# Optimization experiments

Measured on AMD Instinct MI355X. Metric: run time of the kernel, lower is better.

## Reference

```python
import jax, jax.numpy as jnp
import numpy as np

E = 8          # num_experts
K = 2          # top_k
CAPF = 1.25    # capacity_factor


def setup_inputs() -> dict:
    key = jax.random.key(0)
    ks = jax.random.split(key, 6)
    B, T, C = 4, 2048, 1024
    x = jax.random.normal(ks[0], (B, T, C), jnp.float32)
    noise = jax.random.normal(ks[1], (B, T, E), jnp.float32)  # stands in for torch.randn_like
    Wr = jax.random.normal(ks[2], (C, E), jnp.float32) * 0.02   # topkroute_linear
    Wn = jax.random.normal(ks[3], (C, E), jnp.float32) * 0.02   # noise_linear
    W1 = jax.random.normal(ks[4], (E, C, 4 * C), jnp.float32) * 0.02  # expert up-proj
    W2 = jax.random.normal(ks[5], (E, 4 * C, C), jnp.float32) * 0.02  # expert down-proj
    return {"x": x, "noise": noise, "Wr": Wr, "Wn": Wn, "W1": W1, "W2": W2}


def reference(x, noise, Wr, Wn, W1, W2):
    B, T, C = x.shape
    N = B * T
    cap = int(N * K / E * CAPF)  # expert_capacity (static)

    # --- NoisyTopkRouter ---
    logits = x @ Wr                                  # [B,T,E]
    noise_logits = x @ Wn                            # [B,T,E]
    noisy = logits + noise * jax.nn.softplus(noise_logits)
    _, idx = jax.lax.top_k(noisy, K)                 # [B,T,K]
    mask_bte = (idx[..., None] == jnp.arange(E)).any(axis=-2)       # [B,T,E]
    gating = jax.nn.softmax(jnp.where(mask_bte, noisy, -jnp.inf), axis=-1)

    flat_x = x.reshape(N, C)
    flat_g = gating.reshape(N, E)

    # --- capacity-limited dispatch (token order, first `cap` per expert) ---
    mask = mask_bte.reshape(N, E).T                  # [E,N]
    rank = jnp.cumsum(mask, axis=1) - 1              # position within expert
    keep = mask & (rank < cap)
    slot = jnp.where(keep, rank, cap)                # overflow -> dump slot `cap`
    tok = jnp.where(keep, jnp.arange(N)[None, :], N) # dropped -> pad token `N`
    s2t = jnp.full((E, cap + 1), N, dtype=jnp.int32)
    s2t = s2t.at[jnp.arange(E)[:, None], slot].set(tok.astype(jnp.int32))[:, :cap]  # [E,cap]

    # --- gather, grouped GEMM (Linear-SiLU-Linear), weight, scatter-add ---
    x_pad = jnp.concatenate([flat_x, jnp.zeros((1, C), flat_x.dtype)], axis=0)
    xin = x_pad[s2t]                                 # [E,cap,C]
    h = jax.nn.silu(jnp.einsum('enc,ech->enh', xin, W1))
    out = jnp.einsum('enh,ehc->enc', h, W2)          # [E,cap,C]
    g_pad = jnp.concatenate([flat_g, jnp.zeros((1, E), flat_g.dtype)], axis=0)
    gate = g_pad[s2t, jnp.arange(E)[:, None]]        # [E,cap]
    weighted = out * gate[..., None]
    upd = jnp.zeros((N + 1, C), x.dtype).at[s2t.reshape(-1)].add(weighted.reshape(-1, C))
    return upd[:N].reshape(B, T, C)
```

## Files before the change

kernel.cpp:

```cpp
#include <hip/hip_runtime.h>
#include <hip/hip_bf16.h>
#include <math.h>

#define C_DIM 1024
#define H_DIM 4096
#define E_NUM 8

typedef __bf16 bf16x8 __attribute__((ext_vector_type(8)));
typedef float f32x4 __attribute__((ext_vector_type(4)));

__device__ __forceinline__ unsigned short f2bf(float f) {
  union { float f; unsigned u; } v; v.f = f;
  unsigned r = v.u + 0x7FFFu + ((v.u >> 16) & 1u);
  return (unsigned short)(r >> 16);
}

__device__ __forceinline__ void gload16(const short* g, short* l) {
  __builtin_amdgcn_global_load_lds(
      (const __attribute__((address_space(1))) unsigned int*)g,
      (__attribute__((address_space(3))) unsigned int*)l, 16, 0, 0);
}

__global__ __launch_bounds__(256) void router_kernel(
    const float* __restrict__ x, const float* __restrict__ noise,
    const float* __restrict__ Wr, const float* __restrict__ Wn,
    int2* __restrict__ idx_out, float2* __restrict__ gate_out, int N)
{
  int t = blockIdx.x;
  int tid = threadIdx.x;
  const float* xrow = x + (size_t)t * C_DIM;
  float accR[E_NUM], accN[E_NUM];
#pragma unroll
  for (int e = 0; e < E_NUM; e++) { accR[e] = 0.f; accN[e] = 0.f; }
  for (int c = tid; c < C_DIM; c += 256) {
    float xv = xrow[c];
    const float* wr = Wr + (size_t)c * E_NUM;
    const float* wn = Wn + (size_t)c * E_NUM;
#pragma unroll
    for (int e = 0; e < E_NUM; e++) {
      accR[e] = fmaf(xv, wr[e], accR[e]);
      accN[e] = fmaf(xv, wn[e], accN[e]);
    }
  }
#pragma unroll
  for (int e = 0; e < E_NUM; e++) {
    for (int off = 32; off > 0; off >>= 1) {
      accR[e] += __shfl_down(accR[e], off, 64);
      accN[e] += __shfl_down(accN[e], off, 64);
    }
  }
  __shared__ float red[4][2 * E_NUM];
  int lane = tid & 63, wave = tid >> 6;
  if (lane == 0) {
#pragma unroll
    for (int e = 0; e < E_NUM; e++) { red[wave][e] = accR[e]; red[wave][E_NUM + e] = accN[e]; }
  }
  __syncthreads();
  if (tid == 0) {
    float ns[E_NUM];
#pragma unroll
    for (int e = 0; e < E_NUM; e++) {
      float lg = red[0][e] + red[1][e] + red[2][e] + red[3][e];
      float nl = red[0][E_NUM + e] + red[1][E_NUM + e] + red[2][E_NUM + e] + red[3][E_NUM + e];
      float sp = fmaxf(nl, 0.f) + log1pf(expf(-fabsf(nl)));
      ns[e] = lg + noise[(size_t)t * E_NUM + e] * sp;
    }
    int i1 = 0; float m1 = ns[0];
    int i2 = -1; float m2 = -INFINITY;
#pragma unroll
    for (int e = 1; e < E_NUM; e++) {
      float v = ns[e];
      if (v > m1) { m2 = m1; i2 = i1; m1 = v; i1 = e; }
      else if (v > m2) { m2 = v; i2 = e; }
    }
    float e2 = expf(m2 - m1);
    float s = 1.f + e2;
    gate_out[t] = make_float2(1.f / s, e2 / s);
    idx_out[t] = make_int2(i1, i2);
  }
}

__global__ __launch_bounds__(256) void scan_kernel(
    const int2* __restrict__ idx, const float2* __restrict__ gates,
    int* __restrict__ s2t, float* __restrict__ gslot, int N, int cap)
{
  int e = blockIdx.x;
  int tid = threadIdx.x;
  for (int s = tid; s < cap; s += 256) { s2t[(size_t)e * cap + s] = N; gslot[(size_t)e * cap + s] = 0.f; }
  __syncthreads();
  __shared__ int wtot[4];
  int lane = tid & 63, wave = tid >> 6;
  int running = 0;
  for (int base = 0; base < N; base += 256) {
    int t = base + tid;
    int2 ix = idx[t];
    bool flag = (ix.x == e) || (ix.y == e);
    unsigned long long m = __ballot(flag);
    int rank = __popcll(m & ((1ull << lane) - 1ull));
    if (lane == 0) wtot[wave] = __popcll(m);
    __syncthreads();
    int woff = 0;
    for (int w = 0; w < wave; w++) woff += wtot[w];
    int slot = running + woff + rank;
    if (flag && slot < cap) {
      s2t[(size_t)e * cap + slot] = t;
      gslot[(size_t)e * cap + slot] = (ix.x == e) ? gates[t].x : gates[t].y;
    }
    running += wtot[0] + wtot[1] + wtot[2] + wtot[3];
    __syncthreads();
  }
}

__global__ __launch_bounds__(256) void convert_x_kernel(
    const float* __restrict__ src, short* __restrict__ dst, int n8)
{
  int i = blockIdx.x * 256 + threadIdx.x;
  if (i >= n8) return;
  const float4* s = (const float4*)src + (size_t)i * 2;
  float4 a = s[0], b = s[1];
  union { unsigned short us[8]; uint4 v; } o;
  o.us[0] = f2bf(a.x); o.us[1] = f2bf(a.y); o.us[2] = f2bf(a.z); o.us[3] = f2bf(a.w);
  o.us[4] = f2bf(b.x); o.us[5] = f2bf(b.y); o.us[6] = f2bf(b.z); o.us[7] = f2bf(b.w);
  ((uint4*)dst)[i] = o.v;
}

__global__ __launch_bounds__(256) void transpose_convert_kernel(
    const float* __restrict__ src, short* __restrict__ dst,
    int R, int Cc, int eBase)
{
  src += (size_t)(eBase + blockIdx.z) * R * Cc;
  dst += (size_t)blockIdx.z * (size_t)R * Cc;
  __shared__ float tile[64][65];
  int c0 = blockIdx.x * 64, r0 = blockIdx.y * 64;
  int tid = threadIdx.x;
  int tr = tid >> 4, tc = (tid & 15) * 4;
#pragma unroll
  for (int p = 0; p < 4; p++) {
    int r = p * 16 + tr;
    float4 v = *(const float4*)(src + (size_t)(r0 + r) * Cc + c0 + tc);
    tile[r][tc] = v.x; tile[r][tc + 1] = v.y; tile[r][tc + 2] = v.z; tile[r][tc + 3] = v.w;
  }
  __syncthreads();
#pragma unroll
  for (int p = 0; p < 4; p++) {
    int c = p * 16 + tr;
    union { unsigned short us[4]; ushort4 v; } o;
#pragma unroll
    for (int j = 0; j < 4; j++) o.us[j] = f2bf(tile[tc + j][c]);
    *(ushort4*)(dst + (size_t)(c0 + c) * R + r0 + tc) = o.v;
  }
}

__global__ __launch_bounds__(256) void mlp1_kernel(
    const short* __restrict__ xbf, const short* __restrict__ W1t,
    const int* __restrict__ s2t, short* __restrict__ h,
    int eBase, int cap, int N)
{
  int ez = blockIdx.z;
  int e = eBase + ez;
  const short* Wt = W1t + (size_t)ez * C_DIM * H_DIM;
  short* hE = h + (size_t)ez * (size_t)cap * H_DIM;
  int row0 = blockIdx.y * 128;
  int col0 = blockIdx.x * 128;
  int tid = threadIdx.x;
  int w = tid >> 6, lane = tid & 63;

  __shared__ short As[4096];
  __shared__ short Bs[4096];

  int tokA = min(s2t[(size_t)e * cap + row0 + lane], N - 1);
  int tokB = min(s2t[(size_t)e * cap + row0 + 64 + lane], N - 1);
  const short* pA0 = xbf + (size_t)tokA * C_DIM + w * 8;
  const short* pA1 = xbf + (size_t)tokB * C_DIM + w * 8;
  const short* pB0 = Wt + (size_t)(col0 + lane) * C_DIM + w * 8;
  const short* pB1 = Wt + (size_t)(col0 + 64 + lane) * C_DIM + w * 8;
  short* lA0 = &As[w * 1024];
  short* lA1 = &As[w * 1024 + 512];
  short* lB0 = &Bs[w * 1024];
  short* lB1 = &Bs[w * 1024 + 512];

  int wr = w >> 1, wc = w & 1;
  int fr = lane & 15, fb = lane >> 4;
  int aoff = (fb * 128 + wr * 64 + fr) * 8;
  int boff = (fb * 128 + wc * 64 + fr) * 8;

  f32x4 acc[4][4];
#pragma unroll
  for (int m = 0; m < 4; m++)
#pragma unroll
    for (int n = 0; n < 4; n++) acc[m][n] = 0.f;

  for (int k0 = 0; k0 < C_DIM; k0 += 32) {
    gload16(pA0 + k0, lA0);
    gload16(pA1 + k0, lA1);
    gload16(pB0 + k0, lB0);
    gload16(pB1 + k0, lB1);
    __syncthreads();
    bf16x8 af[4], bg[4];
#pragma unroll
    for (int m = 0; m < 4; m++) af[m] = *(const bf16x8*)&As[aoff + m * 128];
#pragma unroll
    for (int n = 0; n < 4; n++) bg[n] = *(const bf16x8*)&Bs[boff + n * 128];
#pragma unroll
    for (int m = 0; m < 4; m++)
#pragma unroll
      for (int n = 0; n < 4; n++)
        acc[m][n] = __builtin_amdgcn_mfma_f32_16x16x32_bf16(af[m], bg[n], acc[m][n], 0, 0, 0);
    __syncthreads();
  }
  int orow = row0 + wr * 64 + fb * 4;
  int ocol = col0 + wc * 64 + fr;
#pragma unroll
  for (int m = 0; m < 4; m++)
#pragma unroll
    for (int r = 0; r < 4; r++) {
      size_t rbase = (size_t)(orow + m * 16 + r) * H_DIM + ocol;
#pragma unroll
      for (int n = 0; n < 4; n++) {
        float v = acc[m][n][r];
        hE[rbase + n * 16] = (short)f2bf(v / (1.f + expf(-v)));
      }
    }
}

__global__ __launch_bounds__(256) void mlp2_kernel(
    const short* __restrict__ h, const short* __restrict__ W2t,
    const int* __restrict__ s2t, const float* __restrict__ gslot,
    float* __restrict__ out, int eBase, int cap, int N)
{
  int ez = blockIdx.z;
  int e = eBase + ez;
  const short* A = h + (size_t)ez * (size_t)cap * H_DIM;
  const short* Wt = W2t + (size_t)ez * C_DIM * H_DIM;
  int row0 = blockIdx.y * 128;
  int col0 = blockIdx.x * 128;
  int tid = threadIdx.x;
  int w = tid >> 6, lane = tid & 63;

  __shared__ short As[4096];
  __shared__ short Bs[4096];

  const short* pA0 = A + (size_t)(row0 + lane) * H_DIM + w * 8;
  const short* pA1 = A + (size_t)(row0 + 64 + lane) * H_DIM + w * 8;
  const short* pB0 = Wt + (size_t)(col0 + lane) * H_DIM + w * 8;
  const short* pB1 = Wt + (size_t)(col0 + 64 + lane) * H_DIM + w * 8;
  short* lA0 = &As[w * 1024];
  short* lA1 = &As[w * 1024 + 512];
  short* lB0 = &Bs[w * 1024];
  short* lB1 = &Bs[w * 1024 + 512];

  int wr = w >> 1, wc = w & 1;
  int fr = lane & 15, fb = lane >> 4;
  int aoff = (fb * 128 + wr * 64 + fr) * 8;
  int boff = (fb * 128 + wc * 64 + fr) * 8;

  f32x4 acc[4][4];
#pragma unroll
  for (int m = 0; m < 4; m++)
#pragma unroll
    for (int n = 0; n < 4; n++) acc[m][n] = 0.f;

  for (int k0 = 0; k0 < H_DIM; k0 += 32) {
    gload16(pA0 + k0, lA0);
    gload16(pA1 + k0, lA1);
    gload16(pB0 + k0, lB0);
    gload16(pB1 + k0, lB1);
    __syncthreads();
    bf16x8 af[4], bg[4];
#pragma unroll
    for (int m = 0; m < 4; m++) af[m] = *(const bf16x8*)&As[aoff + m * 128];
#pragma unroll
    for (int n = 0; n < 4; n++) bg[n] = *(const bf16x8*)&Bs[boff + n * 128];
#pragma unroll
    for (int m = 0; m < 4; m++)
#pragma unroll
      for (int n = 0; n < 4; n++)
        acc[m][n] = __builtin_amdgcn_mfma_f32_16x16x32_bf16(af[m], bg[n], acc[m][n], 0, 0, 0);
    __syncthreads();
  }
  int ocol = col0 + wc * 64 + fr;
#pragma unroll
  for (int m = 0; m < 4; m++)
#pragma unroll
    for (int r = 0; r < 4; r++) {
      int slot = row0 + wr * 64 + m * 16 + fb * 4 + r;
      int tok = s2t[(size_t)e * cap + slot];
      if (tok < N) {
        float g = gslot[(size_t)e * cap + slot];
        float* op = out + (size_t)tok * C_DIM + ocol;
#pragma unroll
        for (int n = 0; n < 4; n++)
          atomicAdd(op + n * 16, g * acc[m][n][r]);
      }
    }
}

extern "C" void kernel_launch(void* const* d_in, const int* in_sizes, int n_in,
                              void* d_out, int out_size, void* d_ws, size_t ws_size,
                              hipStream_t stream)
{
  const float* x     = (const float*)d_in[0];
  const float* noise = (const float*)d_in[1];
  const float* Wr    = (const float*)d_in[2];
  const float* Wn    = (const float*)d_in[3];
  const float* W1    = (const float*)d_in[4];
  const float* W2    = (const float*)d_in[5];
  float* out = (float*)d_out;

  int N = in_sizes[0] / C_DIM;
  int cap = (int)((double)N * 2.0 / E_NUM * 1.25);

  size_t off = 0;
  auto alloc = [&](size_t bytes) -> char* {
    char* r = (char*)d_ws + off;
    off += (bytes + 255) & ~(size_t)255;
    return r;
  };
  int2*   idx   = (int2*)alloc((size_t)N * sizeof(int2));
  float2* gates = (float2*)alloc((size_t)N * sizeof(float2));
  int*    s2t   = (int*)alloc((size_t)E_NUM * cap * sizeof(int));
  float*  gslot = (float*)alloc((size_t)E_NUM * cap * sizeof(float));
  short*  xbf   = (short*)alloc((size_t)N * C_DIM * sizeof(short));
  size_t fixed = off;

  size_t wBytes = (size_t)C_DIM * H_DIM * sizeof(short);
  size_t hBytes = (size_t)cap * H_DIM * sizeof(short);
  size_t perE = 2 * ((wBytes + 255) & ~(size_t)255) + ((hBytes + 255) & ~(size_t)255);
  int g = (ws_size > fixed) ? (int)((ws_size - fixed) / perE) : 1;
  if (g < 1) g = 1;
  if (g > E_NUM) g = E_NUM;
  short* W1t = (short*)alloc((size_t)g * wBytes);
  short* W2t = (short*)alloc((size_t)g * wBytes);
  short* h   = (short*)alloc((size_t)g * hBytes);

  hipMemsetAsync(d_out, 0, (size_t)out_size * sizeof(float), stream);
  router_kernel<<<N, 256, 0, stream>>>(x, noise, Wr, Wn, idx, gates, N);
  scan_kernel<<<E_NUM, 256, 0, stream>>>(idx, gates, s2t, gslot, N, cap);
  convert_x_kernel<<<(N * C_DIM / 8 + 255) / 256, 256, 0, stream>>>(x, xbf, N * C_DIM / 8);

  for (int eb = 0; eb < E_NUM; eb += g) {
    int ge = min(g, E_NUM - eb);
    transpose_convert_kernel<<<dim3(H_DIM / 64, C_DIM / 64, ge), 256, 0, stream>>>(
        W1, W1t, C_DIM, H_DIM, eb);
    transpose_convert_kernel<<<dim3(C_DIM / 64, H_DIM / 64, ge), 256, 0, stream>>>(
        W2, W2t, H_DIM, C_DIM, eb);
    mlp1_kernel<<<dim3(H_DIM / 128, cap / 128, ge), 256, 0, stream>>>(
        xbf, W1t, s2t, h, eb, cap, N);
    mlp2_kernel<<<dim3(C_DIM / 128, cap / 128, ge), 256, 0, stream>>>(
        h, W2t, s2t, gslot, out, eb, cap, N);
  }
}
```

Baseline: 903.5 us.

## Replace MoE GEMMs with pipelined 256x256 tiled kernel, split-K, and count-based skipping

Merges the two expert GEMM kernels into one templated kernel. It uses 256x256 tiles with 512 threads, a four-buffer LDS pipeline with explicit vmcnt waits and setprio, and XCD-aware block swizzling. Workgroups whose row range lies past an expert's actual token count exit early. The second GEMM is split four ways along K, relying on the existing atomic scatter-add. Weight transposes now run for all experts at once instead of in workspace-limited groups, which needs more workspace and assumes cap is divisible by 256.

```diff
diff --git a/kernel.cpp b/kernel.cpp
--- a/kernel.cpp
+++ b/kernel.cpp
@@ -82,7 +82,8 @@
 
 __global__ __launch_bounds__(256) void scan_kernel(
     const int2* __restrict__ idx, const float2* __restrict__ gates,
-    int* __restrict__ s2t, float* __restrict__ gslot, int N, int cap)
+    int* __restrict__ s2t, float* __restrict__ gslot, int* __restrict__ counts,
+    int N, int cap)
 {
   int e = blockIdx.x;
   int tid = threadIdx.x;
@@ -109,6 +110,7 @@
     running += wtot[0] + wtot[1] + wtot[2] + wtot[3];
     __syncthreads();
   }
+  if (tid == 0) counts[e] = min(running, cap);
 }
 
 __global__ __launch_bounds__(256) void convert_x_kernel(
@@ -126,9 +128,9 @@
 
 __global__ __launch_bounds__(256) void transpose_convert_kernel(
     const float* __restrict__ src, short* __restrict__ dst,
-    int R, int Cc, int eBase)
-{
-  src += (size_t)(eBase + blockIdx.z) * R * Cc;
+    int R, int Cc)
+{
+  src += (size_t)blockIdx.z * R * Cc;
   dst += (size_t)blockIdx.z * (size_t)R * Cc;
   __shared__ float tile[64][65];
   int c0 = blockIdx.x * 64, r0 = blockIdx.y * 64;
@@ -151,148 +153,154 @@
   }
 }
 
-__global__ __launch_bounds__(256) void mlp1_kernel(
-    const short* __restrict__ xbf, const short* __restrict__ W1t,
-    const int* __restrict__ s2t, short* __restrict__ h,
-    int eBase, int cap, int N)
-{
-  int ez = blockIdx.z;
-  int e = eBase + ez;
-  const short* Wt = W1t + (size_t)ez * C_DIM * H_DIM;
-  short* hE = h + (size_t)ez * (size_t)cap * H_DIM;
-  int row0 = blockIdx.y * 128;
-  int col0 = blockIdx.x * 128;
+#define TILE_SH 8192
+
+template<int MODE>
+__global__ __launch_bounds__(512, 2) void gemm_moe(
+    const short* __restrict__ Abase, const short* __restrict__ Wt,
+    const int* __restrict__ s2t, const float* __restrict__ gslot,
+    const int* __restrict__ counts, void* __restrict__ outp,
+    int cap, int N, int rows)
+{
+  __shared__ short As[4 * TILE_SH];
+  __shared__ short Bs[4 * TILE_SH];
+
+  int nwg = gridDim.x;
+  int cpx = nwg >> 3;
+  int flat = blockIdx.x;
+  int swz = (flat & 7) * cpx + (flat >> 3);
+
+  int row, col, e, kc;
+  if (MODE == 0) {
+    row = swz % rows; int tmp = swz / rows;
+    col = tmp & 15; e = tmp >> 4; kc = 0;
+  } else {
+    row = swz % rows; int tmp = swz / rows;
+    col = tmp & 3; tmp >>= 2;
+    kc = tmp & 3; e = tmp >> 2;
+  }
+  int cnt = counts[e];
+  int row0 = row * 256;
+  if (row0 >= cnt) return;
+  int col0 = col * 256;
+
   int tid = threadIdx.x;
-  int w = tid >> 6, lane = tid & 63;
-
-  __shared__ short As[4096];
-  __shared__ short Bs[4096];
-
-  int tokA = min(s2t[(size_t)e * cap + row0 + lane], N - 1);
-  int tokB = min(s2t[(size_t)e * cap + row0 + 64 + lane], N - 1);
-  const short* pA0 = xbf + (size_t)tokA * C_DIM + w * 8;
-  const short* pA1 = xbf + (size_t)tokB * C_DIM + w * 8;
-  const short* pB0 = Wt + (size_t)(col0 + lane) * C_DIM + w * 8;
-  const short* pB1 = Wt + (size_t)(col0 + 64 + lane) * C_DIM + w * 8;
-  short* lA0 = &As[w * 1024];
-  short* lA1 = &As[w * 1024 + 512];
-  short* lB0 = &Bs[w * 1024];
-  short* lB1 = &Bs[w * 1024 + 512];
-
-  int wr = w >> 1, wc = w & 1;
-  int fr = lane & 15, fb = lane >> 4;
-  int aoff = (fb * 128 + wr * 64 + fr) * 8;
-  int boff = (fb * 128 + wc * 64 + fr) * 8;
-
-  f32x4 acc[4][4];
-#pragma unroll
-  for (int m = 0; m < 4; m++)
+  int w = tid >> 6, l = tid & 63;
+  int wr = w >> 2, wc = w & 3;
+  int srow = (w & 3) * 64 + l;
+  int ko0 = (w >> 2) * 8;
+  int ko1 = (2 + (w >> 2)) * 8;
+  int ld0 = (w * 64 + l) * 8;
+  int ld1 = (512 + w * 64 + l) * 8;
+
+  const short* gA;
+  const short* gB;
+  if (MODE == 0) {
+    int tok = s2t[(size_t)e * cap + row0 + srow];
+    if (tok >= N) tok = N - 1;
+    gA = Abase + (size_t)tok * C_DIM;
+    gB = Wt + (size_t)e * (C_DIM * H_DIM) + (size_t)(col0 + srow) * C_DIM;
+  } else {
+    gA = Abase + ((size_t)e * cap + row0 + srow) * H_DIM + kc * 1024;
+    gB = Wt + (size_t)e * (C_DIM * H_DIM) + (size_t)(col0 + srow) * H_DIM + kc * 1024;
+  }
+  const int KT = 32;
+
+  int aBase = ((l >> 4) * 256 + wr * 128 + (l & 15)) * 8;
+  int bBase = ((l >> 4) * 256 + wc * 64 + (l & 15)) * 8;
+
+  f32x4 acc[8][4];
+#pragma unroll
+  for (int m = 0; m < 8; m++)
 #pragma unroll
     for (int n = 0; n < 4; n++) acc[m][n] = 0.f;
 
-  for (int k0 = 0; k0 < C_DIM; k0 += 32) {
-    gload16(pA0 + k0, lA0);
-    gload16(pA1 + k0, lA1);
-    gload16(pB0 + k0, lB0);
-    gload16(pB1 + k0, lB1);
-    __syncthreads();
-    bf16x8 af[4], bg[4];
-#pragma unroll
-    for (int m = 0; m < 4; m++) af[m] = *(const bf16x8*)&As[aoff + m * 128];
-#pragma unroll
-    for (int n = 0; n < 4; n++) bg[n] = *(const bf16x8*)&Bs[boff + n * 128];
+#pragma unroll
+  for (int t = 0; t < 3; ++t) {
+    int boff = t * TILE_SH;
+    gload16(gA + t * 32 + ko0, &As[boff + ld0]);
+    gload16(gA + t * 32 + ko1, &As[boff + ld1]);
+    gload16(gB + t * 32 + ko0, &Bs[boff + ld0]);
+    gload16(gB + t * 32 + ko1, &Bs[boff + ld1]);
+  }
+
+#pragma unroll 1
+  for (int t = 0; t < KT; ++t) {
+    if (t < KT - 2)       asm volatile("s_waitcnt vmcnt(8)" ::: "memory");
+    else if (t == KT - 2) asm volatile("s_waitcnt vmcnt(4)" ::: "memory");
+    else                  asm volatile("s_waitcnt vmcnt(0)" ::: "memory");
+    __builtin_amdgcn_s_barrier();
+    __builtin_amdgcn_sched_barrier(0);
+
+    int bufc = (t & 3) * TILE_SH;
+    int tp = t + 3;
+    int bufp = (tp & 3) * TILE_SH;
+    bool st = tp < KT;
+
+    if (st) {
+      gload16(gA + tp * 32 + ko0, &As[bufp + ld0]);
+      gload16(gA + tp * 32 + ko1, &As[bufp + ld1]);
+    }
+    bf16x8 bfr[4], afr[4];
+#pragma unroll
+    for (int n = 0; n < 4; n++) bfr[n] = *(const bf16x8*)&Bs[bufc + bBase + n * 128];
+#pragma unroll
+    for (int m = 0; m < 4; m++) afr[m] = *(const bf16x8*)&As[bufc + aBase + m * 128];
+    __builtin_amdgcn_s_setprio(1);
 #pragma unroll
     for (int m = 0; m < 4; m++)
 #pragma unroll
       for (int n = 0; n < 4; n++)
-        acc[m][n] = __builtin_amdgcn_mfma_f32_16x16x32_bf16(af[m], bg[n], acc[m][n], 0, 0, 0);
-    __syncthreads();
-  }
-  int orow = row0 + wr * 64 + fb * 4;
-  int ocol = col0 + wc * 64 + fr;
-#pragma unroll
-  for (int m = 0; m < 4; m++)
-#pragma unroll
-    for (int r = 0; r < 4; r++) {
-      size_t rbase = (size_t)(orow + m * 16 + r) * H_DIM + ocol;
-#pragma unroll
-      for (int n = 0; n < 4; n++) {
-        float v = acc[m][n][r];
-        hE[rbase + n * 16] = (short)f2bf(v / (1.f + expf(-v)));
+        acc[m][n] = __builtin_amdgcn_mfma_f32_16x16x32_bf16(afr[m], bfr[n], acc[m][n], 0, 0, 0);
+    __builtin_amdgcn_s_setprio(0);
+
+    if (st) {
+      gload16(gB + tp * 32 + ko0, &Bs[bufp + ld0]);
+      gload16(gB + tp * 32 + ko1, &Bs[bufp + ld1]);
+    }
+#pragma unroll
+    for (int m = 0; m < 4; m++) afr[m] = *(const bf16x8*)&As[bufc + aBase + (m + 4) * 128];
+    __builtin_amdgcn_s_setprio(1);
+#pragma unroll
+    for (int m = 0; m < 4; m++)
+#pragma unroll
+      for (int n = 0; n < 4; n++)
+        acc[m + 4][n] = __builtin_amdgcn_mfma_f32_16x16x32_bf16(afr[m], bfr[n], acc[m + 4][n], 0, 0, 0);
+    __builtin_amdgcn_s_setprio(0);
+  }
+
+  int orow = row0 + wr * 128 + (l >> 4) * 4;
+  int ocol = col0 + wc * 64 + (l & 15);
+  if (MODE == 0) {
+    short* hE = (short*)outp + (size_t)e * cap * H_DIM;
+#pragma unroll
+    for (int m = 0; m < 8; m++)
+#pragma unroll
+      for (int r = 0; r < 4; r++) {
+        size_t rb = (size_t)(orow + m * 16 + r) * H_DIM + ocol;
+#pragma unroll
+        for (int n = 0; n < 4; n++) {
+          float v = acc[m][n][r];
+          hE[rb + n * 16] = (short)f2bf(v / (1.f + expf(-v)));
+        }
       }
-    }
-}
-
-__global__ __launch_bounds__(256) void mlp2_kernel(
-    const short* __restrict__ h, const short* __restrict__ W2t,
-    const int* __restrict__ s2t, const float* __restrict__ gslot,
-    float* __restrict__ out, int eBase, int cap, int N)
-{
-  int ez = blockIdx.z;
-  int e = eBase + ez;
-  const short* A = h + (size_t)ez * (size_t)cap * H_DIM;
-  const short* Wt = W2t + (size_t)ez * C_DIM * H_DIM;
-  int row0 = blockIdx.y * 128;
-  int col0 = blockIdx.x * 128;
-  int tid = threadIdx.x;
-  int w = tid >> 6, lane = tid & 63;
-
-  __shared__ short As[4096];
-  __shared__ short Bs[4096];
-
-  const short* pA0 = A + (size_t)(row0 + lane) * H_DIM + w * 8;
-  const short* pA1 = A + (size_t)(row0 + 64 + lane) * H_DIM + w * 8;
-  const short* pB0 = Wt + (size_t)(col0 + lane) * H_DIM + w * 8;
-  const short* pB1 = Wt + (size_t)(col0 + 64 + lane) * H_DIM + w * 8;
-  short* lA0 = &As[w * 1024];
-  short* lA1 = &As[w * 1024 + 512];
-  short* lB0 = &Bs[w * 1024];
-  short* lB1 = &Bs[w * 1024 + 512];
-
-  int wr = w >> 1, wc = w & 1;
-  int fr = lane & 15, fb = lane >> 4;
-  int aoff = (fb * 128 + wr * 64 + fr) * 8;
-  int boff = (fb * 128 + wc * 64 + fr) * 8;
-
-  f32x4 acc[4][4];
-#pragma unroll
-  for (int m = 0; m < 4; m++)
-#pragma unroll
-    for (int n = 0; n < 4; n++) acc[m][n] = 0.f;
-
-  for (int k0 = 0; k0 < H_DIM; k0 += 32) {
-    gload16(pA0 + k0, lA0);
-    gload16(pA1 + k0, lA1);
-    gload16(pB0 + k0, lB0);
-    gload16(pB1 + k0, lB1);
-    __syncthreads();
-    bf16x8 af[4], bg[4];
-#pragma unroll
-    for (int m = 0; m < 4; m++) af[m] = *(const bf16x8*)&As[aoff + m * 128];
-#pragma unroll
-    for (int n = 0; n < 4; n++) bg[n] = *(const bf16x8*)&Bs[boff + n * 128];
-#pragma unroll
-    for (int m = 0; m < 4; m++)
-#pragma unroll
-      for (int n = 0; n < 4; n++)
-        acc[m][n] = __builtin_amdgcn_mfma_f32_16x16x32_bf16(af[m], bg[n], acc[m][n], 0, 0, 0);
-    __syncthreads();
-  }
-  int ocol = col0 + wc * 64 + fr;
-#pragma unroll
-  for (int m = 0; m < 4; m++)
-#pragma unroll
-    for (int r = 0; r < 4; r++) {
-      int slot = row0 + wr * 64 + m * 16 + fb * 4 + r;
-      int tok = s2t[(size_t)e * cap + slot];
-      if (tok < N) {
-        float g = gslot[(size_t)e * cap + slot];
-        float* op = out + (size_t)tok * C_DIM + ocol;
-#pragma unroll
-        for (int n = 0; n < 4; n++)
-          atomicAdd(op + n * 16, g * acc[m][n][r]);
+  } else {
+    float* out = (float*)outp;
+#pragma unroll
+    for (int m = 0; m < 8; m++)
+#pragma unroll
+      for (int r = 0; r < 4; r++) {
+        int slot = row0 + wr * 128 + m * 16 + (l >> 4) * 4 + r;
+        int tok = s2t[(size_t)e * cap + slot];
+        if (tok < N) {
+          float g = gslot[(size_t)e * cap + slot];
+          float* op = out + (size_t)tok * C_DIM + ocol;
+#pragma unroll
+          for (int n = 0; n < 4; n++)
+            atomicAdd(op + n * 16, g * acc[m][n][r]);
+        }
       }
-    }
+  }
 }
 
 extern "C" void kernel_launch(void* const* d_in, const int* in_sizes, int n_in,
@@ -309,6 +317,7 @@
 
   int N = in_sizes[0] / C_DIM;
   int cap = (int)((double)N * 2.0 / E_NUM * 1.25);
+  int rows = cap / 256;
 
   size_t off = 0;
   auto alloc = [&](size_t bytes) -> char* {
@@ -316,37 +325,28 @@
     off += (bytes + 255) & ~(size_t)255;
     return r;
   };
-  int2*   idx   = (int2*)alloc((size_t)N * sizeof(int2));
-  float2* gates = (float2*)alloc((size_t)N * sizeof(float2));
-  int*    s2t   = (int*)alloc((size_t)E_NUM * cap * sizeof(int));
-  float*  gslot = (float*)alloc((size_t)E_NUM * cap * sizeof(float));
-  short*  xbf   = (short*)alloc((size_t)N * C_DIM * sizeof(short));
-  size_t fixed = off;
-
-  size_t wBytes = (size_t)C_DIM * H_DIM * sizeof(short);
-  size_t hBytes = (size_t)cap * H_DIM * sizeof(short);
-  size_t perE = 2 * ((wBytes + 255) & ~(size_t)255) + ((hBytes + 255) & ~(size_t)255);
-  int g = (ws_size > fixed) ? (int)((ws_size - fixed) / perE) : 1;
-  if (g < 1) g = 1;
-  if (g > E_NUM) g = E_NUM;
-  short* W1t = (short*)alloc((size_t)g * wBytes);
-  short* W2t = (short*)alloc((size_t)g * wBytes);
-  short* h   = (short*)alloc((size_t)g * hBytes);
+  int2*   idx    = (int2*)alloc((size_t)N * sizeof(int2));
+  float2* gates  = (float2*)alloc((size_t)N * sizeof(float2));
+  int*    s2t    = (int*)alloc((size_t)E_NUM * cap * sizeof(int));
+  float*  gslot  = (float*)alloc((size_t)E_NUM * cap * sizeof(float));
+  int*    counts = (int*)alloc(E_NUM * sizeof(int));
+  short*  xbf    = (short*)alloc((size_t)N * C_DIM * sizeof(short));
+  short*  W1t    = (short*)alloc((size_t)E_NUM * C_DIM * H_DIM * sizeof(short));
+  short*  W2t    = (short*)alloc((size_t)E_NUM * C_DIM * H_DIM * sizeof(short));
+  short*  h      = (short*)alloc((size_t)E_NUM * cap * H_DIM * sizeof(short));
+  (void)ws_size;
 
   hipMemsetAsync(d_out, 0, (size_t)out_size * sizeof(float), stream);
   router_kernel<<<N, 256, 0, stream>>>(x, noise, Wr, Wn, idx, gates, N);
-  scan_kernel<<<E_NUM, 256, 0, stream>>>(idx, gates, s2t, gslot, N, cap);
+  scan_kernel<<<E_NUM, 256, 0, stream>>>(idx, gates, s2t, gslot, counts, N, cap);
   convert_x_kernel<<<(N * C_DIM / 8 + 255) / 256, 256, 0, stream>>>(x, xbf, N * C_DIM / 8);
-
-  for (int eb = 0; eb < E_NUM; eb += g) {
-    int ge = min(g, E_NUM - eb);
-    transpose_convert_kernel<<<dim3(H_DIM / 64, C_DIM / 64, ge), 256, 0, stream>>>(
-        W1, W1t, C_DIM, H_DIM, eb);
-    transpose_convert_kernel<<<dim3(C_DIM / 64, H_DIM / 64, ge), 256, 0, stream>>>(
-        W2, W2t, H_DIM, C_DIM, eb);
-    mlp1_kernel<<<dim3(H_DIM / 128, cap / 128, ge), 256, 0, stream>>>(
-        xbf, W1t, s2t, h, eb, cap, N);
-    mlp2_kernel<<<dim3(C_DIM / 128, cap / 128, ge), 256, 0, stream>>>(
-        h, W2t, s2t, gslot, out, eb, cap, N);
-  }
-}
+  transpose_convert_kernel<<<dim3(H_DIM / 64, C_DIM / 64, E_NUM), 256, 0, stream>>>(
+      W1, W1t, C_DIM, H_DIM);
+  transpose_convert_kernel<<<dim3(C_DIM / 64, H_DIM / 64, E_NUM), 256, 0, stream>>>(
+      W2, W2t, H_DIM, C_DIM);
+
+  gemm_moe<0><<<dim3(16 * rows * E_NUM), 512, 0, stream>>>(
+      xbf, W1t, s2t, gslot, counts, h, cap, N, rows);
+  gemm_moe<1><<<dim3(4 * rows * 4 * E_NUM), 512, 0, stream>>>(
+      h, W2t, s2t, gslot, counts, out, cap, N, rows);
+}
```

Measured after the change: 865.7 us. 4.2% less time.
